# Kernel optimization log

Measured on AMD Instinct MI355X. Metric: run time of the kernel, lower is better.

## Reference

```python
import jax, jax.numpy as jnp
import numpy as np

N, E, C, H, L, G, K, NC = 50000, 500000, 256, 128, 4, 64, 8, 2
EPS_MSG = 1e-7  # GENConv message eps
EPS_BN = 1e-5   # BatchNorm eps


def setup_inputs() -> dict:
    key = jax.random.key(0)
    ks = jax.random.split(key, 32)
    def nrm(k, shape, scale):
        return jax.random.normal(k, shape, dtype=jnp.float32) * scale
    sC = 1.0 / np.sqrt(C).astype(np.float32)
    sH = 1.0 / np.sqrt(H).astype(np.float32)
    s2H = 1.0 / np.sqrt(2 * H).astype(np.float32)
    return dict(
        x=nrm(ks[0], (N, C), 1.0),
        edge_index=jax.random.randint(ks[1], (2, E), 0, N, dtype=jnp.int32),
        edge_attr=jax.random.uniform(ks[2], (E, 1), dtype=jnp.float32),
        batch=jnp.sort(jax.random.randint(ks[3], (N,), 0, G, dtype=jnp.int32)),
        clinical=nrm(ks[4], (G, K), 1.0),
        lin_src_w=nrm(ks[5], (C, H), sC), lin_src_b=nrm(ks[6], (H,), 0.01),
        lin_dst_w=nrm(ks[7], (C, H), sC), lin_dst_b=nrm(ks[8], (H,), 0.01),
        edge_w=nrm(ks[9], (L, 1, H), 1.0), edge_b=nrm(ks[10], (L, H), 0.01),
        t=0.1 + 0.01 * jax.random.normal(ks[11], (L,), dtype=jnp.float32),
        mlp_w1=nrm(ks[12], (L, H, 2 * H), sH), mlp_b1=nrm(ks[13], (L, 2 * H), 0.01),
        mlp_bn_g=1.0 + nrm(ks[14], (L, 2 * H), 0.1), mlp_bn_b=nrm(ks[15], (L, 2 * H), 0.1),
        mlp_bn_m=nrm(ks[16], (L, 2 * H), 0.1),
        mlp_bn_v=1.0 + jax.random.uniform(ks[17], (L, 2 * H), dtype=jnp.float32),
        mlp_w2=nrm(ks[18], (L, 2 * H, H), s2H), mlp_b2=nrm(ks[19], (L, H), 0.01),
        norm_g=1.0 + nrm(ks[20], (L, H), 0.1), norm_b=nrm(ks[21], (L, H), 0.1),
        norm_m=nrm(ks[22], (L, H), 0.1),
        norm_v=1.0 + jax.random.uniform(ks[23], (L, H), dtype=jnp.float32),
        cls_w=nrm(ks[24], (H + K, NC), 1.0 / np.sqrt(H + K).astype(np.float32)),
        cls_b=nrm(ks[25], (NC,), 0.01),
    )


def _bn(h, g, b, m, v):
    # eval-mode BatchNorm with running stats
    return g * (h - m) * jax.lax.rsqrt(v + EPS_BN) + b


def reference(x, edge_index, edge_attr, batch, clinical,
              lin_src_w, lin_src_b, lin_dst_w, lin_dst_b,
              edge_w, edge_b, t,
              mlp_w1, mlp_b1, mlp_bn_g, mlp_bn_b, mlp_bn_m, mlp_bn_v,
              mlp_w2, mlp_b2, norm_g, norm_b, norm_m, norm_v,
              cls_w, cls_b):
    n = x.shape[0]
    g_count = clinical.shape[0]
    src, dst = edge_index[0], edge_index[1]
    n_layers = t.shape[0]

    def genconv(xs, xd, l):
        # xs: source features feeding messages [N,H]; xd: dst skip features [N,H]
        e = edge_attr @ edge_w[l] + edge_b[l]               # [E,H]
        msg = jax.nn.relu(xs[src] + e) + EPS_MSG            # [E,H]
        z = msg * t[l]
        zmax = jax.ops.segment_max(z, dst, num_segments=n)  # [N,H]
        zmax = jnp.where(jnp.isfinite(zmax), zmax, 0.0)
        ez = jnp.exp(z - zmax[dst])
        denom = jax.ops.segment_sum(ez, dst, num_segments=n)
        agg = jax.ops.segment_sum(msg * ez, dst, num_segments=n) / jnp.maximum(denom, 1e-16)
        out = agg + xd
        # internal MLP [H, 2H, H]: Linear -> BN -> ReLU -> Linear
        hmid = jax.nn.relu(_bn(out @ mlp_w1[l] + mlp_b1[l],
                               mlp_bn_g[l], mlp_bn_b[l], mlp_bn_m[l], mlp_bn_v[l]))
        return hmid @ mlp_w2[l] + mlp_b2[l]

    # layer 0: conv only (per DeepGCN.forward); lin_src / lin_dst project C -> H
    xs0 = x @ lin_src_w + lin_src_b
    xd0 = x @ lin_dst_w + lin_dst_b
    h = genconv(xs0, xd0, 0)

    # layers 1..L-1: res+ block (norm -> act -> conv, residual add); dropout = identity (eval)
    for l in range(1, n_layers):
        r = jax.nn.relu(_bn(h, norm_g[l], norm_b[l], norm_m[l], norm_v[l]))
        h = h + genconv(r, r, l)

    # final norm/act from layer 0
    h = jax.nn.relu(_bn(h, norm_g[0], norm_b[0], norm_m[0], norm_v[0]))

    # global mean pool over graphs
    cnt = jax.ops.segment_sum(jnp.ones((n,), h.dtype), batch, num_segments=g_count)
    pooled = jax.ops.segment_sum(h, batch, num_segments=g_count) / jnp.maximum(cnt, 1.0)[:, None]

    z = jnp.concatenate([pooled, clinical], axis=1)
    return z @ cls_w + cls_b  # [G, num_classes]; squeeze is a no-op for G>1, NC=2
```

## Files before the change

kernel.cpp:

```cpp
#include <hip/hip_runtime.h>
#include <math.h>

#define Nn 50000
#define MPAD 50048
#define Ee 500000
#define Cc 256
#define Hh 128
#define Ll 4
#define Gg 64
#define Kk 8
#define NCc 2

#define NB 196

typedef __attribute__((ext_vector_type(8))) short short8;
typedef __attribute__((ext_vector_type(4))) float f32x4;
typedef __attribute__((ext_vector_type(2))) float f32x2;

#define RFL __builtin_amdgcn_readfirstlane

__device__ __forceinline__ unsigned short f2bf(float f) {
    union { float f; unsigned int u; } v;
    v.f = f;
    unsigned int u = v.u;
    return (unsigned short)((u + 0x7FFFu + ((u >> 16) & 1u)) >> 16);
}
__device__ __forceinline__ float bf2f(unsigned short s) {
    union { float f; unsigned int u; } v;
    v.u = ((unsigned int)s) << 16;
    return v.f;
}
__device__ __forceinline__ float bf2f_lo(unsigned int u) {
    union { float f; unsigned int u; } v;
    v.u = u << 16;
    return v.f;
}
__device__ __forceinline__ float bf2f_hi(unsigned int u) {
    union { float f; unsigned int u; } v;
    v.u = u & 0xffff0000u;
    return v.f;
}


__global__ void hist_kernel(const int* __restrict__ dst, int* __restrict__ deg) {
    int e = blockIdx.x * 256 + threadIdx.x;
    if (e < Ee) atomicAdd(&deg[dst[e]], 1);
}

__global__ __launch_bounds__(256) void bsum_kernel(const int* __restrict__ deg,
                                                   int* __restrict__ bsum) {
    __shared__ int ws[4];
    int t = threadIdx.x;
    int i = blockIdx.x * 256 + t;
    int v = (i < Nn) ? deg[i] : 0;
#pragma unroll
    for (int o = 32; o; o >>= 1) v += __shfl_down(v, o, 64);
    if ((t & 63) == 0) ws[t >> 6] = v;
    __syncthreads();
    if (t == 0) bsum[blockIdx.x] = ws[0] + ws[1] + ws[2] + ws[3];
}

__global__ __launch_bounds__(256) void bscan_kernel(const int* __restrict__ bsum,
                                                    int* __restrict__ boff,
                                                    int* __restrict__ off) {
    __shared__ int sc[256];
    int t = threadIdx.x;
    int v = (t < NB) ? bsum[t] : 0;
    sc[t] = v;
    __syncthreads();
    for (int o = 1; o < 256; o <<= 1) {
        int u = (t >= o) ? sc[t - o] : 0;
        __syncthreads();
        sc[t] += u;
        __syncthreads();
    }
    if (t < NB) boff[t] = sc[t] - v;
    if (t == NB - 1) off[Nn] = sc[t];
}

__global__ __launch_bounds__(256) void offsets_kernel(const int* __restrict__ deg,
                                                      const int* __restrict__ boff,
                                                      int* __restrict__ off,
                                                      int* __restrict__ pos) {
    __shared__ int sc[256];
    int t = threadIdx.x;
    int i = blockIdx.x * 256 + t;
    int v = (i < Nn) ? deg[i] : 0;
    sc[t] = v;
    __syncthreads();
    for (int o = 1; o < 256; o <<= 1) {
        int u = (t >= o) ? sc[t - o] : 0;
        __syncthreads();
        sc[t] += u;
        __syncthreads();
    }
    int excl = sc[t] - v + boff[blockIdx.x];
    if (i < Nn) {
        off[i] = excl;
        pos[i] = excl;
    }
}

__global__ void scatter_kernel(const int* __restrict__ src, const int* __restrict__ dst,
                               const float* __restrict__ attr, int* __restrict__ pos,
                               int2* __restrict__ sedge) {
    int e = blockIdx.x * 256 + threadIdx.x;
    if (e < Ee) {
        int d = dst[e];
        int p = atomicAdd(&pos[d], 1);
        sedge[p] = make_int2(src[e], __float_as_int(attr[e]));
    }
}


__global__ void wconv_kernel(const float* __restrict__ lin_src_w,
                             const float* __restrict__ lin_dst_w,
                             const float* __restrict__ mlp_w1,
                             const float* __restrict__ mlp_w2,
                             unsigned short* __restrict__ wt) {
    int idx = blockIdx.x * 256 + threadIdx.x;
    if (idx >= 327680) return;
    float val;
    if (idx < 65536) {
        int n = idx >> 8, k = idx & 255;
        val = (n < 128) ? lin_src_w[k * 128 + n] : lin_dst_w[k * 128 + (n - 128)];
    } else if (idx < 196608) {
        int r = idx - 65536;
        int l = r >> 15, e = r & 32767;
        int n = e >> 7, k = e & 127;
        val = mlp_w1[(size_t)l * 32768 + k * 256 + n];
    } else {
        int r = idx - 196608;
        int l = r >> 15, e = r & 32767;
        int n = e >> 8, k = e & 255;
        val = mlp_w2[(size_t)l * 32768 + k * 128 + n];
    }
    wt[idx] = f2bf(val);
}


__global__ __launch_bounds__(256) void xconv_kernel(const float* __restrict__ x,
                                                    unsigned short* __restrict__ xbf) {
    int idx = blockIdx.x * 256 + threadIdx.x;
    if (idx >= (Nn * Cc) / 8) return;
    const float4* p = (const float4*)(x) + (size_t)idx * 2;
    float4 v0 = p[0], v1 = p[1];
    unsigned short t[8];
    t[0] = f2bf(v0.x); t[1] = f2bf(v0.y); t[2] = f2bf(v0.z); t[3] = f2bf(v0.w);
    t[4] = f2bf(v1.x); t[5] = f2bf(v1.y); t[6] = f2bf(v1.z); t[7] = f2bf(v1.w);
    *(short8*)(xbf + (size_t)idx * 8) = *(short8*)t;
}

#define GLOAD16(gp, lp)                                                                       \
    __builtin_amdgcn_global_load_lds(                                                         \
        (const __attribute__((address_space(1))) unsigned int*)(gp),                          \
        (__attribute__((address_space(3))) unsigned int*)(lp), 16, 0, 0)


__global__ __launch_bounds__(256) void proj_kernel(
    const unsigned short* __restrict__ A, const unsigned short* __restrict__ Bt,
    const float* __restrict__ bias, const float* __restrict__ bias2,
    unsigned short* __restrict__ Cout) {
    __shared__ __align__(16) unsigned short SH[24576];
    int tid = threadIdx.x;
    int wave = tid >> 6, lane = tid & 63;
    int wr = wave >> 1, wc = wave & 1;
    int lrow = lane & 15, quad = lane >> 4;
    int m0 = blockIdx.y * 128, n0 = blockIdx.x * 128;
    const int K = 256;

    const unsigned short* ag0 = A + (size_t)(m0 + (tid >> 2)) * K + (tid & 3) * 8;
    const unsigned short* ag1 = A + (size_t)(m0 + 64 + (tid >> 2)) * K + (tid & 3) * 8;
    const unsigned short* bg0 = Bt + (size_t)(n0 + (tid >> 2)) * K + (tid & 3) * 8;
    const unsigned short* bg1 = Bt + (size_t)(n0 + 64 + (tid >> 2)) * K + (tid & 3) * 8;

    f32x4 acc[4][4];
#pragma unroll
    for (int i = 0; i < 4; i++)
#pragma unroll
        for (int j = 0; j < 4; j++) acc[i][j] = (f32x4){0.f, 0.f, 0.f, 0.f};

    auto stage = [&](int buf, int koff) {
        GLOAD16(ag0 + koff, SH + buf * 4096 + wave * 512);
        GLOAD16(ag1 + koff, SH + buf * 4096 + 2048 + wave * 512);
        GLOAD16(bg0 + koff, SH + 12288 + buf * 4096 + wave * 512);
        GLOAD16(bg1 + koff, SH + 12288 + buf * 4096 + 2048 + wave * 512);
    };

    const int ntiles = 8;
    stage(0, 0);
    stage(1, 32);
    for (int t = 0; t < ntiles; ++t) {
        if (t + 1 < ntiles) {
            asm volatile("s_waitcnt vmcnt(4)\n\ts_barrier" ::: "memory");
        } else {
            asm volatile("s_waitcnt vmcnt(0)\n\ts_barrier" ::: "memory");
        }
        if (t + 2 < ntiles) stage((t + 2) % 3, (t + 2) * 32);
        int cur = t % 3;
        const unsigned short* As = SH + cur * 4096;
        const unsigned short* Bs = SH + 12288 + cur * 4096;
        short8 af[4], bfr[4];
#pragma unroll
        for (int mt = 0; mt < 4; mt++)
            af[mt] = *(const short8*)&As[(wr * 64 + mt * 16 + lrow) * 32 + quad * 8];
#pragma unroll
        for (int nf = 0; nf < 4; nf++)
            bfr[nf] = *(const short8*)&Bs[(wc * 64 + nf * 16 + lrow) * 32 + quad * 8];
#pragma unroll
        for (int mt = 0; mt < 4; mt++)
#pragma unroll
            for (int nf = 0; nf < 4; nf++)
                acc[mt][nf] = __builtin_amdgcn_mfma_f32_16x16x32_bf16(af[mt], bfr[nf],
                                                                     acc[mt][nf], 0, 0, 0);
    }

    __syncthreads();
    unsigned short* Cl = SH;
#pragma unroll
    for (int nf = 0; nf < 4; nf++) {
        int gc = n0 + wc * 64 + nf * 16 + lrow;
        float bs = (gc >= 128) ? bias2[gc - 128] : bias[gc];
        int col = wc * 64 + nf * 16 + lrow;
#pragma unroll
        for (int mt = 0; mt < 4; mt++)
#pragma unroll
            for (int r = 0; r < 4; r++)
                Cl[(wr * 64 + mt * 16 + quad * 4 + r) * 128 + col] = f2bf(acc[mt][nf][r] + bs);
    }
    __syncthreads();
#pragma unroll
    for (int p = 0; p < 8; p++) {
        int vid = p * 256 + tid;
        int row = vid >> 4, cg = (vid & 15) * 8;
        short8 v = *(const short8*)&Cl[row * 128 + cg];
        *(short8*)(Cout + (size_t)(m0 + row) * 256 + n0 + cg) = v;
    }
}


__global__ __launch_bounds__(256) void mlp_kernel(
    const unsigned short* __restrict__ A,
    const unsigned short* __restrict__ W1,
    const unsigned short* __restrict__ W2,
    const float* __restrict__ b1, const float* __restrict__ bn_g,
    const float* __restrict__ bn_b, const float* __restrict__ bn_m,
    const float* __restrict__ bn_v, const float* __restrict__ b2,
    const float* __restrict__ pn_g, const float* __restrict__ pn_b,
    const float* __restrict__ pn_m, const float* __restrict__ pn_v,
    float* __restrict__ hbuf, unsigned short* __restrict__ rbuf,
    const int* __restrict__ batch, float* __restrict__ pooled,
    float* __restrict__ cnt, int rmw, int dopool) {
    __shared__ __align__(16) unsigned short S[20480];
    __shared__ __align__(16) unsigned short Hm[64 * 264];

    int tid = threadIdx.x;
    int wave = tid >> 6, lane = tid & 63;
    int lrow = lane & 15, quad = lane >> 4;
    int m0 = blockIdx.x * 64;

    const unsigned short* ag = A + (size_t)(m0 + (tid >> 2)) * 128 + (tid & 3) * 8;
    const unsigned short* bg = W1 + (size_t)(tid >> 2) * 128 + (tid & 3) * 8;

    f32x4 acc1[4][4];
#pragma unroll
    for (int i = 0; i < 4; i++)
#pragma unroll
        for (int j = 0; j < 4; j++) acc1[i][j] = (f32x4){0.f, 0.f, 0.f, 0.f};

    auto stage1 = [&](int buf, int k0) {
        GLOAD16(ag + k0, S + buf * 2048 + wave * 512);
#pragma unroll
        for (int c = 0; c < 4; c++)
            GLOAD16(bg + (size_t)c * 64 * 128 + k0,
                    S + 4096 + buf * 8192 + c * 2048 + wave * 512);
    };

    stage1(0, 0);
    __syncthreads();
    for (int t = 0; t < 4; ++t) {
        if (t + 1 < 4) stage1((t + 1) & 1, (t + 1) * 32);
        int cur = t & 1;
        const unsigned short* A1s = S + cur * 2048;
        const unsigned short* B1s = S + 4096 + cur * 8192;
        short8 af[4], bfr[4];
#pragma unroll
        for (int mt = 0; mt < 4; mt++)
            af[mt] = *(const short8*)&A1s[(mt * 16 + lrow) * 32 + quad * 8];
#pragma unroll
        for (int nf = 0; nf < 4; nf++)
            bfr[nf] = *(const short8*)&B1s[(wave * 64 + nf * 16 + lrow) * 32 + quad * 8];
#pragma unroll
        for (int mt = 0; mt < 4; mt++)
#pragma unroll
            for (int nf = 0; nf < 4; nf++)
                acc1[mt][nf] = __builtin_amdgcn_mfma_f32_16x16x32_bf16(af[mt], bfr[nf],
                                                                      acc1[mt][nf], 0, 0, 0);
        __syncthreads();
    }

#pragma unroll
    for (int nf = 0; nf < 4; nf++) {
        int gc = wave * 64 + nf * 16 + lrow;
        float bs = b1[gc];
        float g = bn_g[gc], bb = bn_b[gc], mm = bn_m[gc];
        float inv = rsqrtf(bn_v[gc] + 1e-5f);
#pragma unroll
        for (int mt = 0; mt < 4; mt++)
#pragma unroll
            for (int r = 0; r < 4; r++) {
                float v = acc1[mt][nf][r] + bs;
                v = fmaxf(g * (v - mm) * inv + bb, 0.f);
                Hm[(mt * 16 + quad * 4 + r) * 264 + gc] = f2bf(v);
            }
    }
    __syncthreads();

    const unsigned short* b2g0 = W2 + (size_t)(tid >> 2) * 256 + (tid & 3) * 8;
    const unsigned short* b2g1 = W2 + (size_t)(64 + (tid >> 2)) * 256 + (tid & 3) * 8;

    f32x4 acc2[4][2];
#pragma unroll
    for (int i = 0; i < 4; i++)
#pragma unroll
        for (int j = 0; j < 2; j++) acc2[i][j] = (f32x4){0.f, 0.f, 0.f, 0.f};

    auto stage2 = [&](int buf, int k0) {
        GLOAD16(b2g0 + k0, S + buf * 4096 + wave * 512);
        GLOAD16(b2g1 + k0, S + buf * 4096 + 2048 + wave * 512);
    };

    stage2(0, 0);
    __syncthreads();
    for (int t = 0; t < 8; ++t) {
        if (t + 1 < 8) stage2((t + 1) & 1, (t + 1) * 32);
        int cur = t & 1;
        const unsigned short* B2s = S + cur * 4096;
        short8 af[4], bfr[2];
#pragma unroll
        for (int mt = 0; mt < 4; mt++)
            af[mt] = *(const short8*)&Hm[(mt * 16 + lrow) * 264 + t * 32 + quad * 8];
#pragma unroll
        for (int nf = 0; nf < 2; nf++)
            bfr[nf] = *(const short8*)&B2s[(wave * 32 + nf * 16 + lrow) * 32 + quad * 8];
#pragma unroll
        for (int mt = 0; mt < 4; mt++)
#pragma unroll
            for (int nf = 0; nf < 2; nf++)
                acc2[mt][nf] = __builtin_amdgcn_mfma_f32_16x16x32_bf16(af[mt], bfr[nf],
                                                                      acc2[mt][nf], 0, 0, 0);
        __syncthreads();
    }

    float* C2 = (float*)S;
    float* PS = (float*)S + 8192;
#pragma unroll
    for (int nf = 0; nf < 2; nf++) {
        int gc = wave * 32 + nf * 16 + lrow;
        float bs = b2[gc];
#pragma unroll
        for (int mt = 0; mt < 4; mt++)
#pragma unroll
            for (int r = 0; r < 4; r++)
                C2[(mt * 16 + quad * 4 + r) * 128 + gc] = acc2[mt][nf][r] + bs;
    }
    if (dopool) {
        for (int f = tid; f < 532; f += 256) PS[f] = 0.f;
    }
    __syncthreads();

    int gfirst = dopool ? RFL(batch[m0]) : 0;
#pragma unroll
    for (int p = 0; p < 8; p++) {
        int vid = p * 256 + tid;
        int row = vid >> 5, c4 = (vid & 31) * 4;
        f32x4 v = *(const f32x4*)&C2[row * 128 + c4];
        float* hp = hbuf + (size_t)(m0 + row) * 128 + c4;
        if (rmw) v += *(const f32x4*)hp;
        if (!dopool) {
            *(f32x4*)hp = v;
            if (pn_g) {
                f32x4 pg = *(const f32x4*)&pn_g[c4];
                f32x4 pb = *(const f32x4*)&pn_b[c4];
                f32x4 pm = *(const f32x4*)&pn_m[c4];
                f32x4 pv = *(const f32x4*)&pn_v[c4];
                float r0 = fmaxf(pg[0] * (v[0] - pm[0]) * rsqrtf(pv[0] + 1e-5f) + pb[0], 0.f);
                float r1 = fmaxf(pg[1] * (v[1] - pm[1]) * rsqrtf(pv[1] + 1e-5f) + pb[1], 0.f);
                float r2 = fmaxf(pg[2] * (v[2] - pm[2]) * rsqrtf(pv[2] + 1e-5f) + pb[2], 0.f);
                float r3 = fmaxf(pg[3] * (v[3] - pm[3]) * rsqrtf(pv[3] + 1e-5f) + pb[3], 0.f);
                unsigned int w0 = (unsigned int)f2bf(r0) | ((unsigned int)f2bf(r1) << 16);
                unsigned int w1 = (unsigned int)f2bf(r2) | ((unsigned int)f2bf(r3) << 16);
                uint2 pk = make_uint2(w0, w1);
                *(uint2*)(rbuf + (size_t)(m0 + row) * 128 + c4) = pk;
            }
        } else if (m0 + row < Nn) {
            f32x4 pg = *(const f32x4*)&pn_g[c4];
            f32x4 pb = *(const f32x4*)&pn_b[c4];
            f32x4 pm = *(const f32x4*)&pn_m[c4];
            f32x4 pv = *(const f32x4*)&pn_v[c4];
            float r0 = fmaxf(pg[0] * (v[0] - pm[0]) * rsqrtf(pv[0] + 1e-5f) + pb[0], 0.f);
            float r1 = fmaxf(pg[1] * (v[1] - pm[1]) * rsqrtf(pv[1] + 1e-5f) + pb[1], 0.f);
            float r2 = fmaxf(pg[2] * (v[2] - pm[2]) * rsqrtf(pv[2] + 1e-5f) + pb[2], 0.f);
            float r3 = fmaxf(pg[3] * (v[3] - pm[3]) * rsqrtf(pv[3] + 1e-5f) + pb[3], 0.f);
            int slot = min(batch[m0 + row] - gfirst, 3);
            float* ps = PS + slot * 132 + c4;
            atomicAdd(ps + 0, r0);
            atomicAdd(ps + 1, r1);
            atomicAdd(ps + 2, r2);
            atomicAdd(ps + 3, r3);
            if ((vid & 31) == 0) atomicAdd(PS + 528 + slot, 1.f);
        }
    }
    if (dopool) {
        __syncthreads();
        for (int f = tid; f < 512; f += 256) {
            int slot = f >> 7, ff = f & 127;
            int gslot = gfirst + slot;
            if (gslot < Gg) atomicAdd(&pooled[gslot * 128 + ff], PS[slot * 132 + ff]);
        }
        if (tid < 4 && gfirst + tid < Gg) atomicAdd(&cnt[gfirst + tid], PS[528 + tid]);
    }
}


template <int XSS>
__global__ __launch_bounds__(256) void agg_kernel(
    const unsigned short* __restrict__ xs,
    const unsigned short* __restrict__ xd, int xds,
    const int2* __restrict__ sedge, const int* __restrict__ off,
    const float* __restrict__ ew, const float* __restrict__ eb,
    const float* __restrict__ tptr, unsigned short* __restrict__ outb) {
    int wave = threadIdx.x >> 6;
    int lane = threadIdx.x & 63;
    int d0 = blockIdx.x * 8 + wave * 2;
    int d1 = d0 + 1;
    int f0 = lane * 2;
    unsigned int uda = *(const unsigned int*)(xd + (size_t)d0 * xds + f0);
    unsigned int udb = *(const unsigned int*)(xd + (size_t)d1 * xds + f0);
    f32x2 wv = *(const f32x2*)(ew + f0);
    f32x2 bv = *(const f32x2*)(eb + f0);
    float c = tptr[0] * 1.44269504088896f;
    const f32x2 zz = {0.f, 0.f};
    int s0a = RFL(off[d0]), s1a = RFL(off[d0 + 1]);
    int s0b = RFL(off[d1]), s1b = RFL(off[d1 + 1]);
    f32x2 dena = {0.f, 0.f}, numa = {0.f, 0.f};
    f32x2 denb = {0.f, 0.f}, numb = {0.f, 0.f};

#define EDGE2(u, av, den, num)                                      \
    {                                                               \
        f32x2 xv = {bf2f_lo(u), bf2f_hi(u)};                        \
        f32x2 m = __builtin_elementwise_max(xv + bv + (av)*wv, zz); \
        f32x2 e;                                                    \
        e.x = __builtin_amdgcn_exp2f(m.x * c);                      \
        e.y = __builtin_amdgcn_exp2f(m.y * c);                      \
        den += e;                                                   \
        num += m * e;                                               \
    }
#define EDGE2M(u, av, mk, den, num)                                 \
    {                                                               \
        f32x2 xv = {bf2f_lo(u), bf2f_hi(u)};                        \
        f32x2 m = __builtin_elementwise_max(xv + bv + (av)*wv, zz); \
        f32x2 e;                                                    \
        e.x = __builtin_amdgcn_exp2f(m.x * c) * (mk);               \
        e.y = __builtin_amdgcn_exp2f(m.y * c) * (mk);               \
        den += e;                                                   \
        num += m * e;                                               \
    }
#define LOADMETA(jv, ii, aa)                                   \
    {                                                          \
        int4 q0 = *(const int4*)(sedge + (jv));                \
        int4 q1 = *(const int4*)(sedge + (jv) + 2);            \
        int4 q2 = *(const int4*)(sedge + (jv) + 4);            \
        int4 q3 = *(const int4*)(sedge + (jv) + 6);            \
        ii[0] = RFL(q0.x); aa[0] = __int_as_float(RFL(q0.y));  \
        ii[1] = RFL(q0.z); aa[1] = __int_as_float(RFL(q0.w));  \
        ii[2] = RFL(q1.x); aa[2] = __int_as_float(RFL(q1.y));  \
        ii[3] = RFL(q1.z); aa[3] = __int_as_float(RFL(q1.w));  \
        ii[4] = RFL(q2.x); aa[4] = __int_as_float(RFL(q2.y));  \
        ii[5] = RFL(q2.z); aa[5] = __int_as_float(RFL(q2.w));  \
        ii[6] = RFL(q3.x); aa[6] = __int_as_float(RFL(q3.y));  \
        ii[7] = RFL(q3.z); aa[7] = __int_as_float(RFL(q3.w));  \
    }
#define GATHER8(ii, uu)                                                          \
    _Pragma("unroll") for (int k = 0; k < 8; k++) uu[k] =                        \
        *(const unsigned int*)(xs + (size_t)ii[k] * XSS + f0);

    int ja = s0a, jb = s0b;
    while (ja + 8 <= s1a && jb + 8 <= s1b) {
        int ia[8], ib[8];
        float aa[8], ab[8];
        LOADMETA(ja, ia, aa)
        LOADMETA(jb, ib, ab)
        unsigned int ua[8], ub[8];
        GATHER8(ia, ua)
        GATHER8(ib, ub)
#pragma unroll
        for (int k = 0; k < 8; k++) EDGE2(ua[k], aa[k], dena, numa)
#pragma unroll
        for (int k = 0; k < 8; k++) EDGE2(ub[k], ab[k], denb, numb)
        ja += 8;
        jb += 8;
    }
    while (ja + 8 <= s1a) {
        int ia[8];
        float aa[8];
        LOADMETA(ja, ia, aa)
        unsigned int ua[8];
        GATHER8(ia, ua)
#pragma unroll
        for (int k = 0; k < 8; k++) EDGE2(ua[k], aa[k], dena, numa)
        ja += 8;
    }
    while (jb + 8 <= s1b) {
        int ib[8];
        float ab[8];
        LOADMETA(jb, ib, ab)
        unsigned int ub[8];
        GATHER8(ib, ub)
#pragma unroll
        for (int k = 0; k < 8; k++) EDGE2(ub[k], ab[k], denb, numb)
        jb += 8;
    }
    if (ja < s1a || jb < s1b) {
        int lasta = (s1a > s0a) ? s1a - 1 : 0;
        int lastb = (s1b > s0b) ? s1b - 1 : 0;
        int ia[8], ib[8];
        float aa[8], ab[8], ma[8], mb[8];
#pragma unroll
        for (int k = 0; k < 8; k++) {
            int jj = ja + k;
            int cl = (jj < s1a) ? jj : lasta;
            int2 p = sedge[cl];
            ia[k] = RFL(p.x);
            aa[k] = __int_as_float(RFL(p.y));
            ma[k] = (jj < s1a) ? 1.f : 0.f;
            jj = jb + k;
            cl = (jj < s1b) ? jj : lastb;
            int2 q = sedge[cl];
            ib[k] = RFL(q.x);
            ab[k] = __int_as_float(RFL(q.y));
            mb[k] = (jj < s1b) ? 1.f : 0.f;
        }
        unsigned int ua[8], ub[8];
        GATHER8(ia, ua)
        GATHER8(ib, ub)
#pragma unroll
        for (int k = 0; k < 8; k++) EDGE2M(ua[k], aa[k], ma[k], dena, numa)
#pragma unroll
        for (int k = 0; k < 8; k++) EDGE2M(ub[k], ab[k], mb[k], denb, numb)
    }
#undef EDGE2
#undef EDGE2M
#undef LOADMETA
#undef GATHER8
    float a0 = (s1a > s0a) ? (numa.x / dena.x + 1e-7f) : 0.f;
    float a1 = (s1a > s0a) ? (numa.y / dena.y + 1e-7f) : 0.f;
    float b0 = (s1b > s0b) ? (numb.x / denb.x + 1e-7f) : 0.f;
    float b1 = (s1b > s0b) ? (numb.y / denb.y + 1e-7f) : 0.f;
    unsigned int lo = f2bf(a0 + bf2f_lo(uda));
    unsigned int hi = f2bf(a1 + bf2f_hi(uda));
    *(unsigned int*)(outb + (size_t)d0 * Hh + f0) = lo | (hi << 16);
    lo = f2bf(b0 + bf2f_lo(udb));
    hi = f2bf(b1 + bf2f_hi(udb));
    *(unsigned int*)(outb + (size_t)d1 * Hh + f0) = lo | (hi << 16);
}


__global__ __launch_bounds__(128) void cls_kernel(const float* __restrict__ pooled,
                                                  const float* __restrict__ cnt,
                                                  const float* __restrict__ clinical,
                                                  const float* __restrict__ w,
                                                  const float* __restrict__ bias,
                                                  float* __restrict__ out) {
    int t = threadIdx.x;
    int g = t >> 1, c = t & 1;
    float inv = 1.f / fmaxf(cnt[g], 1.f);
    float s = bias[c];
    for (int j = 0; j < Hh; j++) s += pooled[g * Hh + j] * inv * w[j * NCc + c];
    for (int k = 0; k < Kk; k++) s += clinical[g * Kk + k] * w[(Hh + k) * NCc + c];
    out[g * NCc + c] = s;
}


extern "C" void kernel_launch(void* const* d_in, const int* in_sizes, int n_in,
                              void* d_out, int out_size, void* d_ws, size_t ws_size,
                              hipStream_t stream) {
    const float* x = (const float*)d_in[0];
    const int* eidx = (const int*)d_in[1];
    const float* eattr = (const float*)d_in[2];
    const int* batch = (const int*)d_in[3];
    const float* clinical = (const float*)d_in[4];
    const float* lin_src_w = (const float*)d_in[5];
    const float* lin_src_b = (const float*)d_in[6];
    const float* lin_dst_w = (const float*)d_in[7];
    const float* lin_dst_b = (const float*)d_in[8];
    const float* edge_w = (const float*)d_in[9];
    const float* edge_b = (const float*)d_in[10];
    const float* tt = (const float*)d_in[11];
    const float* mlp_w1 = (const float*)d_in[12];
    const float* mlp_b1 = (const float*)d_in[13];
    const float* bn_g = (const float*)d_in[14];
    const float* bn_b = (const float*)d_in[15];
    const float* bn_m = (const float*)d_in[16];
    const float* bn_v = (const float*)d_in[17];
    const float* mlp_w2 = (const float*)d_in[18];
    const float* mlp_b2 = (const float*)d_in[19];
    const float* norm_g = (const float*)d_in[20];
    const float* norm_b = (const float*)d_in[21];
    const float* norm_m = (const float*)d_in[22];
    const float* norm_v = (const float*)d_in[23];
    const float* cls_w = (const float*)d_in[24];
    const float* cls_b = (const float*)d_in[25];
    float* out = (float*)d_out;

    const int* src = eidx;
    const int* dst = eidx + Ee;

    char* ws = (char*)d_ws;
    size_t off_b = 0;
    auto alloc = [&](size_t bytes) -> void* {
        void* p = ws + off_b;
        off_b += (bytes + 255) & ~(size_t)255;
        return p;
    };
    unsigned short* xsd = (unsigned short*)alloc((size_t)MPAD * 256 * 2);
    unsigned short* rbuf = (unsigned short*)alloc((size_t)MPAD * Hh * 2);
    unsigned short* aggout = (unsigned short*)alloc((size_t)MPAD * Hh * 2);
    unsigned short* xbf = (unsigned short*)alloc((size_t)MPAD * 256 * 2);
    float* hbuf = (float*)alloc((size_t)MPAD * Hh * 4);
    int* deg = (int*)alloc((Nn + 1) * 4);
    int* offp = (int*)alloc((Nn + 1) * 4);
    int* pos = (int*)alloc((size_t)Nn * 4);
    int* bsum = (int*)alloc(NB * 4);
    int* boff = (int*)alloc(NB * 4);
    int2* sedge = (int2*)alloc((size_t)Ee * 8);
    float* pooled = (float*)alloc((size_t)Gg * Hh * 4);
    float* cntb = (float*)alloc(Gg * 4);
    unsigned short* wt = (unsigned short*)alloc((size_t)327680 * 2);

    hipMemsetAsync(deg, 0, (Nn + 1) * 4, stream);
    hipMemsetAsync(pooled, 0, (size_t)Gg * Hh * 4, stream);
    hipMemsetAsync(cntb, 0, Gg * 4, stream);

    hist_kernel<<<(Ee + 255) / 256, 256, 0, stream>>>(dst, deg);
    bsum_kernel<<<NB, 256, 0, stream>>>(deg, bsum);
    bscan_kernel<<<1, 256, 0, stream>>>(bsum, boff, offp);
    offsets_kernel<<<NB, 256, 0, stream>>>(deg, boff, offp, pos);
    scatter_kernel<<<(Ee + 255) / 256, 256, 0, stream>>>(src, dst, eattr, pos, sedge);
    wconv_kernel<<<1280, 256, 0, stream>>>(lin_src_w, lin_dst_w, mlp_w1, mlp_w2, wt);
    xconv_kernel<<<(Nn * Cc / 8 + 255) / 256, 256, 0, stream>>>(x, xbf);

    const unsigned short* wt_proj = wt;
    const unsigned short* wt_w1 = wt + 65536;
    const unsigned short* wt_w2 = wt + 196608;

    dim3 gproj(2, MPAD / 128);
    proj_kernel<<<gproj, 256, 0, stream>>>(xbf, wt_proj, lin_src_b, lin_dst_b, xsd);

    for (int l = 0; l < Ll; l++) {
        if (l == 0) {
            agg_kernel<256><<<Nn / 8, 256, 0, stream>>>(xsd, xsd + 128, 256, sedge, offp,
                                                        edge_w + l * Hh, edge_b + l * Hh,
                                                        tt + l, aggout);
        } else {
            agg_kernel<128><<<Nn / 8, 256, 0, stream>>>(rbuf, rbuf, Hh, sedge, offp,
                                                        edge_w + l * Hh, edge_b + l * Hh,
                                                        tt + l, aggout);
        }
        int dopool = (l == Ll - 1) ? 1 : 0;
        const float* png = dopool ? norm_g : (norm_g + (l + 1) * Hh);
        const float* pnb = dopool ? norm_b : (norm_b + (l + 1) * Hh);
        const float* pnm = dopool ? norm_m : (norm_m + (l + 1) * Hh);
        const float* pnv = dopool ? norm_v : (norm_v + (l + 1) * Hh);
        mlp_kernel<<<MPAD / 64, 256, 0, stream>>>(
            aggout, wt_w1 + (size_t)l * 32768, wt_w2 + (size_t)l * 32768,
            mlp_b1 + l * 2 * Hh, bn_g + l * 2 * Hh, bn_b + l * 2 * Hh,
            bn_m + l * 2 * Hh, bn_v + l * 2 * Hh, mlp_b2 + l * Hh,
            png, pnb, pnm, pnv, hbuf, rbuf, batch, pooled, cntb,
            (l == 0) ? 0 : 1, dopool);
    }

    cls_kernel<<<1, 128, 0, stream>>>(pooled, cntb, clinical, cls_w, cls_b, out);
}
```

Measured before the change: 501.9 us.

## Load MLP operands directly from global memory and split pooling into separate kernel

```diff
diff --git a/kernel.cpp b/kernel.cpp
--- a/kernel.cpp
+++ b/kernel.cpp
@@ -248,10 +248,7 @@
     const float* __restrict__ bn_v, const float* __restrict__ b2,
     const float* __restrict__ pn_g, const float* __restrict__ pn_b,
     const float* __restrict__ pn_m, const float* __restrict__ pn_v,
-    float* __restrict__ hbuf, unsigned short* __restrict__ rbuf,
-    const int* __restrict__ batch, float* __restrict__ pooled,
-    float* __restrict__ cnt, int rmw, int dopool) {
-    __shared__ __align__(16) unsigned short S[20480];
+    float* __restrict__ hbuf, unsigned short* __restrict__ rbuf, int rmw) {
     __shared__ __align__(16) unsigned short Hm[64 * 264];
 
     int tid = threadIdx.x;
@@ -259,46 +256,29 @@
     int lrow = lane & 15, quad = lane >> 4;
     int m0 = blockIdx.x * 64;
 
-    const unsigned short* ag = A + (size_t)(m0 + (tid >> 2)) * 128 + (tid & 3) * 8;
-    const unsigned short* bg = W1 + (size_t)(tid >> 2) * 128 + (tid & 3) * 8;
-
     f32x4 acc1[4][4];
 #pragma unroll
     for (int i = 0; i < 4; i++)
 #pragma unroll
         for (int j = 0; j < 4; j++) acc1[i][j] = (f32x4){0.f, 0.f, 0.f, 0.f};
-
-    auto stage1 = [&](int buf, int k0) {
-        GLOAD16(ag + k0, S + buf * 2048 + wave * 512);
-#pragma unroll
-        for (int c = 0; c < 4; c++)
-            GLOAD16(bg + (size_t)c * 64 * 128 + k0,
-                    S + 4096 + buf * 8192 + c * 2048 + wave * 512);
-    };
-
-    stage1(0, 0);
-    __syncthreads();
-    for (int t = 0; t < 4; ++t) {
-        if (t + 1 < 4) stage1((t + 1) & 1, (t + 1) * 32);
-        int cur = t & 1;
-        const unsigned short* A1s = S + cur * 2048;
-        const unsigned short* B1s = S + 4096 + cur * 8192;
+#pragma unroll
+    for (int t = 0; t < 4; t++) {
         short8 af[4], bfr[4];
 #pragma unroll
         for (int mt = 0; mt < 4; mt++)
-            af[mt] = *(const short8*)&A1s[(mt * 16 + lrow) * 32 + quad * 8];
+            af[mt] = *(const short8*)(A + (size_t)(m0 + mt * 16 + lrow) * 128 +
+                                      t * 32 + quad * 8);
 #pragma unroll
         for (int nf = 0; nf < 4; nf++)
-            bfr[nf] = *(const short8*)&B1s[(wave * 64 + nf * 16 + lrow) * 32 + quad * 8];
+            bfr[nf] = *(const short8*)(W1 + (size_t)(wave * 64 + nf * 16 + lrow) * 128 +
+                                       t * 32 + quad * 8);
 #pragma unroll
         for (int mt = 0; mt < 4; mt++)
 #pragma unroll
             for (int nf = 0; nf < 4; nf++)
                 acc1[mt][nf] = __builtin_amdgcn_mfma_f32_16x16x32_bf16(af[mt], bfr[nf],
                                                                       acc1[mt][nf], 0, 0, 0);
-        __syncthreads();
-    }
-
+    }
 #pragma unroll
     for (int nf = 0; nf < 4; nf++) {
         int gc = wave * 64 + nf * 16 + lrow;
@@ -316,44 +296,31 @@
     }
     __syncthreads();
 
-    const unsigned short* b2g0 = W2 + (size_t)(tid >> 2) * 256 + (tid & 3) * 8;
-    const unsigned short* b2g1 = W2 + (size_t)(64 + (tid >> 2)) * 256 + (tid & 3) * 8;
-
     f32x4 acc2[4][2];
 #pragma unroll
     for (int i = 0; i < 4; i++)
 #pragma unroll
         for (int j = 0; j < 2; j++) acc2[i][j] = (f32x4){0.f, 0.f, 0.f, 0.f};
-
-    auto stage2 = [&](int buf, int k0) {
-        GLOAD16(b2g0 + k0, S + buf * 4096 + wave * 512);
-        GLOAD16(b2g1 + k0, S + buf * 4096 + 2048 + wave * 512);
-    };
-
-    stage2(0, 0);
-    __syncthreads();
-    for (int t = 0; t < 8; ++t) {
-        if (t + 1 < 8) stage2((t + 1) & 1, (t + 1) * 32);
-        int cur = t & 1;
-        const unsigned short* B2s = S + cur * 4096;
+#pragma unroll
+    for (int t = 0; t < 8; t++) {
         short8 af[4], bfr[2];
 #pragma unroll
         for (int mt = 0; mt < 4; mt++)
             af[mt] = *(const short8*)&Hm[(mt * 16 + lrow) * 264 + t * 32 + quad * 8];
 #pragma unroll
         for (int nf = 0; nf < 2; nf++)
-            bfr[nf] = *(const short8*)&B2s[(wave * 32 + nf * 16 + lrow) * 32 + quad * 8];
+            bfr[nf] = *(const short8*)(W2 + (size_t)(wave * 32 + nf * 16 + lrow) * 256 +
+                                       t * 32 + quad * 8);
 #pragma unroll
         for (int mt = 0; mt < 4; mt++)
 #pragma unroll
             for (int nf = 0; nf < 2; nf++)
                 acc2[mt][nf] = __builtin_amdgcn_mfma_f32_16x16x32_bf16(af[mt], bfr[nf],
                                                                       acc2[mt][nf], 0, 0, 0);
-        __syncthreads();
-    }
-
-    float* C2 = (float*)S;
-    float* PS = (float*)S + 8192;
+    }
+    __syncthreads();
+
+    float* C2 = (float*)Hm;
 #pragma unroll
     for (int nf = 0; nf < 2; nf++) {
         int gc = wave * 32 + nf * 16 + lrow;
@@ -362,38 +329,18 @@
         for (int mt = 0; mt < 4; mt++)
 #pragma unroll
             for (int r = 0; r < 4; r++)
-                C2[(mt * 16 + quad * 4 + r) * 128 + gc] = acc2[mt][nf][r] + bs;
-    }
-    if (dopool) {
-        for (int f = tid; f < 532; f += 256) PS[f] = 0.f;
-    }
-    __syncthreads();
-
-    int gfirst = dopool ? RFL(batch[m0]) : 0;
+                C2[(mt * 16 + quad * 4 + r) * 132 + gc] = acc2[mt][nf][r] + bs;
+    }
+    __syncthreads();
 #pragma unroll
     for (int p = 0; p < 8; p++) {
         int vid = p * 256 + tid;
         int row = vid >> 5, c4 = (vid & 31) * 4;
-        f32x4 v = *(const f32x4*)&C2[row * 128 + c4];
+        f32x4 v = *(const f32x4*)&C2[row * 132 + c4];
         float* hp = hbuf + (size_t)(m0 + row) * 128 + c4;
         if (rmw) v += *(const f32x4*)hp;
-        if (!dopool) {
-            *(f32x4*)hp = v;
-            if (pn_g) {
-                f32x4 pg = *(const f32x4*)&pn_g[c4];
-                f32x4 pb = *(const f32x4*)&pn_b[c4];
-                f32x4 pm = *(const f32x4*)&pn_m[c4];
-                f32x4 pv = *(const f32x4*)&pn_v[c4];
-                float r0 = fmaxf(pg[0] * (v[0] - pm[0]) * rsqrtf(pv[0] + 1e-5f) + pb[0], 0.f);
-                float r1 = fmaxf(pg[1] * (v[1] - pm[1]) * rsqrtf(pv[1] + 1e-5f) + pb[1], 0.f);
-                float r2 = fmaxf(pg[2] * (v[2] - pm[2]) * rsqrtf(pv[2] + 1e-5f) + pb[2], 0.f);
-                float r3 = fmaxf(pg[3] * (v[3] - pm[3]) * rsqrtf(pv[3] + 1e-5f) + pb[3], 0.f);
-                unsigned int w0 = (unsigned int)f2bf(r0) | ((unsigned int)f2bf(r1) << 16);
-                unsigned int w1 = (unsigned int)f2bf(r2) | ((unsigned int)f2bf(r3) << 16);
-                uint2 pk = make_uint2(w0, w1);
-                *(uint2*)(rbuf + (size_t)(m0 + row) * 128 + c4) = pk;
-            }
-        } else if (m0 + row < Nn) {
+        *(f32x4*)hp = v;
+        if (pn_g) {
             f32x4 pg = *(const f32x4*)&pn_g[c4];
             f32x4 pb = *(const f32x4*)&pn_b[c4];
             f32x4 pm = *(const f32x4*)&pn_m[c4];
@@ -402,23 +349,11 @@
             float r1 = fmaxf(pg[1] * (v[1] - pm[1]) * rsqrtf(pv[1] + 1e-5f) + pb[1], 0.f);
             float r2 = fmaxf(pg[2] * (v[2] - pm[2]) * rsqrtf(pv[2] + 1e-5f) + pb[2], 0.f);
             float r3 = fmaxf(pg[3] * (v[3] - pm[3]) * rsqrtf(pv[3] + 1e-5f) + pb[3], 0.f);
-            int slot = min(batch[m0 + row] - gfirst, 3);
-            float* ps = PS + slot * 132 + c4;
-            atomicAdd(ps + 0, r0);
-            atomicAdd(ps + 1, r1);
-            atomicAdd(ps + 2, r2);
-            atomicAdd(ps + 3, r3);
-            if ((vid & 31) == 0) atomicAdd(PS + 528 + slot, 1.f);
+            unsigned int w0 = (unsigned int)f2bf(r0) | ((unsigned int)f2bf(r1) << 16);
+            unsigned int w1 = (unsigned int)f2bf(r2) | ((unsigned int)f2bf(r3) << 16);
+            uint2 pk = make_uint2(w0, w1);
+            *(uint2*)(rbuf + (size_t)(m0 + row) * 128 + c4) = pk;
         }
-    }
-    if (dopool) {
-        __syncthreads();
-        for (int f = tid; f < 512; f += 256) {
-            int slot = f >> 7, ff = f & 127;
-            int gslot = gfirst + slot;
-            if (gslot < Gg) atomicAdd(&pooled[gslot * 128 + ff], PS[slot * 132 + ff]);
-        }
-        if (tid < 4 && gfirst + tid < Gg) atomicAdd(&cnt[gfirst + tid], PS[528 + tid]);
     }
 }
 
@@ -563,6 +498,38 @@
     lo = f2bf(b0 + bf2f_lo(udb));
     hi = f2bf(b1 + bf2f_hi(udb));
     *(unsigned int*)(outb + (size_t)d1 * Hh + f0) = lo | (hi << 16);
+}
+
+
+#define PCHUNK 100
+
+__global__ __launch_bounds__(128) void pool_kernel(
+    const float* __restrict__ h, const int* __restrict__ batch,
+    const float* __restrict__ g, const float* __restrict__ b,
+    const float* __restrict__ m, const float* __restrict__ v,
+    float* __restrict__ pooled, float* __restrict__ cnt) {
+    int hh = threadIdx.x;
+    int i0 = blockIdx.x * PCHUNK;
+    int i1 = min(i0 + PCHUNK, Nn);
+    if (i0 >= Nn) return;
+    float gg = g[hh], bb = b[hh], mm = m[hh], inv = rsqrtf(v[hh] + 1e-5f);
+    int cur = batch[i0];
+    float sum = 0.f, c = 0.f;
+    for (int i = i0; i < i1; i++) {
+        int gid = batch[i];
+        float val = fmaxf(gg * (h[(size_t)i * Hh + hh] - mm) * inv + bb, 0.f);
+        if (gid != cur) {
+            atomicAdd(&pooled[(size_t)cur * Hh + hh], sum);
+            if (hh == 0) atomicAdd(&cnt[cur], c);
+            cur = gid;
+            sum = 0.f;
+            c = 0.f;
+        }
+        sum += val;
+        c += 1.f;
+    }
+    atomicAdd(&pooled[(size_t)cur * Hh + hh], sum);
+    if (hh == 0) atomicAdd(&cnt[cur], c);
 }
 
 
@@ -667,18 +634,18 @@
                                                         edge_w + l * Hh, edge_b + l * Hh,
                                                         tt + l, aggout);
         }
-        int dopool = (l == Ll - 1) ? 1 : 0;
-        const float* png = dopool ? norm_g : (norm_g + (l + 1) * Hh);
-        const float* pnb = dopool ? norm_b : (norm_b + (l + 1) * Hh);
-        const float* pnm = dopool ? norm_m : (norm_m + (l + 1) * Hh);
-        const float* pnv = dopool ? norm_v : (norm_v + (l + 1) * Hh);
+        const float* png = (l < Ll - 1) ? (norm_g + (l + 1) * Hh) : nullptr;
+        const float* pnb = (l < Ll - 1) ? (norm_b + (l + 1) * Hh) : nullptr;
+        const float* pnm = (l < Ll - 1) ? (norm_m + (l + 1) * Hh) : nullptr;
+        const float* pnv = (l < Ll - 1) ? (norm_v + (l + 1) * Hh) : nullptr;
         mlp_kernel<<<MPAD / 64, 256, 0, stream>>>(
             aggout, wt_w1 + (size_t)l * 32768, wt_w2 + (size_t)l * 32768,
             mlp_b1 + l * 2 * Hh, bn_g + l * 2 * Hh, bn_b + l * 2 * Hh,
             bn_m + l * 2 * Hh, bn_v + l * 2 * Hh, mlp_b2 + l * Hh,
-            png, pnb, pnm, pnv, hbuf, rbuf, batch, pooled, cntb,
-            (l == 0) ? 0 : 1, dopool);
-    }
-
+            png, pnb, pnm, pnv, hbuf, rbuf, (l == 0) ? 0 : 1);
+    }
+
+    pool_kernel<<<(Nn + PCHUNK - 1) / PCHUNK, 128, 0, stream>>>(hbuf, batch, norm_g, norm_b,
+                                                                norm_m, norm_v, pooled, cntb);
     cls_kernel<<<1, 128, 0, stream>>>(pooled, cntb, clinical, cls_w, cls_b, out);
 }
```

New measurement: 528.1 us. 5.2% more time.
